# Performance work log

Hardware: AMD Instinct MI355X
Metric: run time of the kernel (lower is better)

Reference implementation:

```python
import jax, jax.numpy as jnp
import numpy as np

R = 6                 # max displacement / padding
D = 2 * R + 1         # window side; D*D = 169 displacements


def setup_inputs() -> dict:
    key = jax.random.key(0)
    k1, k2, k3 = jax.random.split(key, 3)
    b, cf, h, w = 2, 32, 256, 256
    feats_t = jax.random.normal(k1, (b, cf, h, w), jnp.float32)
    feats_r = jax.random.normal(k2, (b, cf, h, w), jnp.float32)
    img_r = jax.random.uniform(k3, (b, 1, h, w), jnp.float32)
    return {"feats_t": feats_t, "feats_r": feats_r, "img_r": img_r}


def _forward(feats_t, feats_r, img_r):
    b, cf, h, w = feats_t.shape
    ci = img_r.shape[1]
    x2p = jnp.pad(feats_r, ((0, 0), (0, 0), (R, R), (R, R)))
    imgp = jnp.pad(img_r, ((0, 0), (0, 0), (R, R), (R, R)))
    # displacement offsets in the same order as the torch double loop (_y outer, _x inner)
    offs = jnp.stack(
        jnp.meshgrid(jnp.arange(D), jnp.arange(D), indexing="ij"), axis=-1
    ).reshape(-1, 2)

    def step(carry, off):
        dy, dx = off[0], off[1]
        win = jax.lax.dynamic_slice(x2p, (0, 0, dy, dx), (b, cf, h, w))
        c = jnp.sum(feats_t * win, axis=1)  # [b, h, w] correlation for this displacement
        iw = jax.lax.dynamic_slice(imgp, (0, 0, dy, dx), (b, ci, h, w))
        return carry, (c, iw)

    _, (corr, imgs) = jax.lax.scan(step, 0, offs)  # corr: [D*D, b, h, w]; imgs: [D*D, b, ci, h, w]
    attn = jax.nn.softmax(corr, axis=0)  # softmax over displacements (torch dim=1 channel axis)
    # weighted sum of shifted reference images -> warped target image
    return jnp.einsum("dbhw,dbchw->bchw", attn, imgs)


def reference(feats_t, feats_r, img_r):
    return _forward(feats_t, feats_r, img_r)
```

## Files before the change

kernel.cpp:

```cpp
#include <hip/hip_runtime.h>
#include <stdint.h>

typedef _Float16 half_t;
typedef _Float16 v4h __attribute__((ext_vector_type(4)));
typedef _Float16 v8h __attribute__((ext_vector_type(8)));
typedef float v4f __attribute__((ext_vector_type(4)));

#define HH 256
#define WW 256
#define HW (HH*WW)
#define TH 32
#define TW 16
#define NROWS (TH+12)
#define NPX   (TW+16)
#define PXS   40
#define RSTEP (NPX*PXS)
#define NTHREADS 1024
#define L2E 1.44269504088896340736f

__global__ __launch_bounds__(NTHREADS, 4)
void corr_recon(const float* __restrict__ ft, const float* __restrict__ fr,
                const float* __restrict__ img, float* __restrict__ out)
{
    __shared__ half_t frl[NROWS * RSTEP];

    const int bid0 = blockIdx.x;
    const int bid  = (bid0 & 7) * 32 + (bid0 >> 3);

    const int b0  = bid >> 7;
    const int rb  = bid & 127;
    const int y0  = (rb >> 4) * TH;
    const int x0t = (rb & 15) * TW;

    const int tid  = threadIdx.x;
    const int lane = tid & 63;
    const int w    = tid >> 6;
    const int n    = lane & 15;
    const int g    = lane >> 4;

    const float* frb = fr  + (size_t)b0 * 32 * HW;
    const float* ftb = ft  + (size_t)b0 * 32 * HW;
    const float* imb = img + (size_t)b0 * HW;

    float iw0r[14], iw1r[14];
    {
        const int gx0  = x0t - 6 + n;
        const int gx1  = gx0 + 16;
        const int gx0c = max(gx0, 0);
        const int gx1c = min(gx1, WW-1);
        const bool okx0 = (gx0 >= 0);
        const bool okx1 = (gx1 < WW);
        #pragma unroll
        for (int u = 0; u < 14; ++u) {
            const int gy  = y0 - 6 + 2*w + u;
            const int gyc = min(max(gy, 0), HH-1);
            const bool oky = (gy == gyc);
            const float v0 = imb[(size_t)gyc * WW + gx0c];
            const float v1 = imb[(size_t)gyc * WW + gx1c];
            iw0r[u] = (oky && okx0) ? v0 : 0.f;
            iw1r[u] = (oky && okx1) ? v1 : 0.f;
        }
    }

    for (int i = tid; i < NROWS * 8 * 8; i += NTHREADS) {
        const int px4 = i & 7;
        const int q   = (i >> 3) & 7;
        const int row = i >> 6;
        const int gy  = y0 - 6 + row;
        const int gx  = x0t - 6 + px4 * 4;
        const int gyc = min(max(gy, 0), HH-1);
        const bool oky = (gy == gyc);
        const float* src = frb + ((size_t)(4*q) * HH + gyc) * WW;
        float t[4][4];
        if (oky && gx >= 0 && gx + 3 < WW) {
            #pragma unroll
            for (int jc = 0; jc < 4; ++jc) {
                float4 v = *(const float4*)(src + (size_t)jc * HW + gx);
                t[jc][0]=v.x; t[jc][1]=v.y; t[jc][2]=v.z; t[jc][3]=v.w;
            }
        } else {
            #pragma unroll
            for (int jc = 0; jc < 4; ++jc)
                #pragma unroll
                for (int e = 0; e < 4; ++e) {
                    int x = gx + e;
                    t[jc][e] = (oky && x >= 0 && x < WW) ? src[(size_t)jc * HW + x] : 0.f;
                }
        }
        const int qo = 8*(q & 3) + 4*(q >> 2);
        #pragma unroll
        for (int jp = 0; jp < 4; ++jp) {
            const int px = px4 * 4 + jp;
            v4h pk;
            pk[0] = (half_t)t[0][jp]; pk[1] = (half_t)t[1][jp];
            pk[2] = (half_t)t[2][jp]; pk[3] = (half_t)t[3][jp];
            *(v4h*)&frl[(row * NPX + px) * PXS + qo] = pk;
        }
    }

    const int y = y0 + 2*w;
    v8h a0, a1;
    {
        const float* fa = ftb + (size_t)y * WW + (x0t + n);
        #pragma unroll
        for (int j = 0; j < 4; ++j) {
            a0[j]   = (half_t)(fa[(size_t)(4*g + j)      * HW] * L2E);
            a0[4+j] = (half_t)(fa[(size_t)(16 + 4*g + j) * HW] * L2E);
            a1[j]   = (half_t)(fa[WW + (size_t)(4*g + j)      * HW] * L2E);
            a1[4+j] = (half_t)(fa[WW + (size_t)(16 + 4*g + j) * HW] * L2E);
        }
    }

    v4f bias0, bias1;
    #pragma unroll
    for (int r = 0; r < 4; ++r) {
        const int m  = 4*g + r;
        const int d0 = n - m;
        const int d1 = 16 + n - m;
        bias0[r] = (d0 >= 0 && d0 <= 12) ? 0.f : -1e4f;
        bias1[r] = (d1 >= 0 && d1 <= 12) ? 0.f : -1e4f;
    }
    const int dm = n - 4*g;

    __syncthreads();

    v4f lp0 = {0,0,0,0}, ap0 = {0,0,0,0};
    v4f lp1 = {0,0,0,0}, ap1 = {0,0,0,0};

    auto STEP = [&](const v8h& a, v4f& lp, v4f& ap,
                    const v8h& B0, const v8h& B1, float iw0, float iw1) {
        v4f c0 = __builtin_amdgcn_mfma_f32_16x16x32_f16(a, B0, bias0, 0, 0, 0);
        v4f c1 = __builtin_amdgcn_mfma_f32_16x16x32_f16(a, B1, bias1, 0, 0, 0);
        #pragma unroll
        for (int r = 0; r < 4; ++r) {
            const bool cond = (dm >= r);
            float cs  = cond ? c0[r] : c1[r];
            float iws = cond ? iw0   : iw1;
            float e = __builtin_amdgcn_exp2f(cs);
            lp[r] += e;
            ap[r] += e * iws;
        }
    };

    const half_t* prd = &frl[(2*w * NPX + n) * PXS + 8*g];
    #pragma unroll
    for (int u = 0; u < 14; ++u) {
        v8h B0 = *(const v8h*)(prd + u*RSTEP);
        v8h B1 = *(const v8h*)(prd + u*RSTEP + 16*PXS);
        if (u <= 12) STEP(a0, lp0, ap0, B0, B1, iw0r[u], iw1r[u]);
        if (u >= 1)  STEP(a1, lp1, ap1, B0, B1, iw0r[u], iw1r[u]);
    }

    #pragma unroll
    for (int r = 0; r < 4; ++r) {
        float l0 = lp0[r], v0 = ap0[r], l1 = lp1[r], v1 = ap1[r];
        l0 += __shfl_xor(l0, 1);  v0 += __shfl_xor(v0, 1);
        l1 += __shfl_xor(l1, 1);  v1 += __shfl_xor(v1, 1);
        l0 += __shfl_xor(l0, 2);  v0 += __shfl_xor(v0, 2);
        l1 += __shfl_xor(l1, 2);  v1 += __shfl_xor(v1, 2);
        l0 += __shfl_xor(l0, 4);  v0 += __shfl_xor(v0, 4);
        l1 += __shfl_xor(l1, 4);  v1 += __shfl_xor(v1, 4);
        l0 += __shfl_xor(l0, 8);  v0 += __shfl_xor(v0, 8);
        l1 += __shfl_xor(l1, 8);  v1 += __shfl_xor(v1, 8);
        lp0[r] = l0; ap0[r] = v0; lp1[r] = l1; ap1[r] = v1;
    }
    if (n < 4) {
        const float l0 = n==0 ? lp0[0] : n==1 ? lp0[1] : n==2 ? lp0[2] : lp0[3];
        const float v0 = n==0 ? ap0[0] : n==1 ? ap0[1] : n==2 ? ap0[2] : ap0[3];
        const float l1 = n==0 ? lp1[0] : n==1 ? lp1[1] : n==2 ? lp1[2] : lp1[3];
        const float v1 = n==0 ? ap1[0] : n==1 ? ap1[1] : n==2 ? ap1[2] : ap1[3];
        float* orow = out + (size_t)b0 * HW + (size_t)y * WW + x0t + 4*g + n;
        orow[0]  = v0 / l0;
        orow[WW] = v1 / l1;
    }
}

extern "C" void kernel_launch(void* const* d_in, const int* in_sizes, int n_in,
                              void* d_out, int out_size, void* d_ws, size_t ws_size,
                              hipStream_t stream)
{
    const float* ft  = (const float*)d_in[0];
    const float* fr  = (const float*)d_in[1];
    const float* img = (const float*)d_in[2];
    float* out = (float*)d_out;
    (void)in_sizes; (void)n_in; (void)out_size; (void)d_ws; (void)ws_size;
    corr_recon<<<256, NTHREADS, 0, stream>>>(ft, fr, img, out);
}
```

Baseline: 19.56 us.

## Drop LDS staging of reference features and load MFMA operands from global memory

Removes the shared-memory tile of fp16 reference features and the block barrier. Each lane now fetches its MFMA B operands straight from global memory, with scalar loads per channel and a cast to fp16 in registers. The tile shrinks to 16 rows with 512 threads, and the grid doubles to 512 blocks to raise parallelism. This avoids the LDS fill and the sync, but it issues many uncoalesced, strided global loads that get re-read across waves and rely on the caches.

```diff
diff --git a/kernel.cpp b/kernel.cpp
--- a/kernel.cpp
+++ b/kernel.cpp
@@ -2,33 +2,26 @@
 #include <stdint.h>
 
 typedef _Float16 half_t;
-typedef _Float16 v4h __attribute__((ext_vector_type(4)));
 typedef _Float16 v8h __attribute__((ext_vector_type(8)));
 typedef float v4f __attribute__((ext_vector_type(4)));
 
 #define HH 256
 #define WW 256
 #define HW (HH*WW)
-#define TH 32
+#define TH 16
 #define TW 16
-#define NROWS (TH+12)
-#define NPX   (TW+16)
-#define PXS   40
-#define RSTEP (NPX*PXS)
-#define NTHREADS 1024
+#define NTHREADS 512
 #define L2E 1.44269504088896340736f
 
 __global__ __launch_bounds__(NTHREADS, 4)
 void corr_recon(const float* __restrict__ ft, const float* __restrict__ fr,
                 const float* __restrict__ img, float* __restrict__ out)
 {
-    __shared__ half_t frl[NROWS * RSTEP];
+    const int bid0 = blockIdx.x;
+    const int bid  = (bid0 & 7) * 64 + (bid0 >> 3);
 
-    const int bid0 = blockIdx.x;
-    const int bid  = (bid0 & 7) * 32 + (bid0 >> 3);
-
-    const int b0  = bid >> 7;
-    const int rb  = bid & 127;
+    const int b0  = bid >> 8;
+    const int rb  = bid & 255;
     const int y0  = (rb >> 4) * TH;
     const int x0t = (rb & 15) * TW;
 
@@ -42,60 +35,23 @@
     const float* ftb = ft  + (size_t)b0 * 32 * HW;
     const float* imb = img + (size_t)b0 * HW;
 
+    const int gx0  = x0t - 6 + n;
+    const int gx1  = gx0 + 16;
+    const int gx0c = max(gx0, 0);
+    const int gx1c = min(gx1, WW-1);
+    const bool okx0 = (gx0 >= 0);
+    const bool okx1 = (gx1 < WW);
+
     float iw0r[14], iw1r[14];
-    {
-        const int gx0  = x0t - 6 + n;
-        const int gx1  = gx0 + 16;
-        const int gx0c = max(gx0, 0);
-        const int gx1c = min(gx1, WW-1);
-        const bool okx0 = (gx0 >= 0);
-        const bool okx1 = (gx1 < WW);
-        #pragma unroll
-        for (int u = 0; u < 14; ++u) {
-            const int gy  = y0 - 6 + 2*w + u;
-            const int gyc = min(max(gy, 0), HH-1);
-            const bool oky = (gy == gyc);
-            const float v0 = imb[(size_t)gyc * WW + gx0c];
-            const float v1 = imb[(size_t)gyc * WW + gx1c];
-            iw0r[u] = (oky && okx0) ? v0 : 0.f;
-            iw1r[u] = (oky && okx1) ? v1 : 0.f;
-        }
-    }
-
-    for (int i = tid; i < NROWS * 8 * 8; i += NTHREADS) {
-        const int px4 = i & 7;
-        const int q   = (i >> 3) & 7;
-        const int row = i >> 6;
-        const int gy  = y0 - 6 + row;
-        const int gx  = x0t - 6 + px4 * 4;
+    #pragma unroll
+    for (int u = 0; u < 14; ++u) {
+        const int gy  = y0 + 2*w - 6 + u;
         const int gyc = min(max(gy, 0), HH-1);
         const bool oky = (gy == gyc);
-        const float* src = frb + ((size_t)(4*q) * HH + gyc) * WW;
-        float t[4][4];
-        if (oky && gx >= 0 && gx + 3 < WW) {
-            #pragma unroll
-            for (int jc = 0; jc < 4; ++jc) {
-                float4 v = *(const float4*)(src + (size_t)jc * HW + gx);
-                t[jc][0]=v.x; t[jc][1]=v.y; t[jc][2]=v.z; t[jc][3]=v.w;
-            }
-        } else {
-            #pragma unroll
-            for (int jc = 0; jc < 4; ++jc)
-                #pragma unroll
-                for (int e = 0; e < 4; ++e) {
-                    int x = gx + e;
-                    t[jc][e] = (oky && x >= 0 && x < WW) ? src[(size_t)jc * HW + x] : 0.f;
-                }
-        }
-        const int qo = 8*(q & 3) + 4*(q >> 2);
-        #pragma unroll
-        for (int jp = 0; jp < 4; ++jp) {
-            const int px = px4 * 4 + jp;
-            v4h pk;
-            pk[0] = (half_t)t[0][jp]; pk[1] = (half_t)t[1][jp];
-            pk[2] = (half_t)t[2][jp]; pk[3] = (half_t)t[3][jp];
-            *(v4h*)&frl[(row * NPX + px) * PXS + qo] = pk;
-        }
+        const float v0 = imb[(size_t)gyc * WW + gx0c];
+        const float v1 = imb[(size_t)gyc * WW + gx1c];
+        iw0r[u] = (oky && okx0) ? v0 : 0.f;
+        iw1r[u] = (oky && okx1) ? v1 : 0.f;
     }
 
     const int y = y0 + 2*w;
@@ -122,8 +78,6 @@
     }
     const int dm = n - 4*g;
 
-    __syncthreads();
-
     v4f lp0 = {0,0,0,0}, ap0 = {0,0,0,0};
     v4f lp1 = {0,0,0,0}, ap1 = {0,0,0,0};
 
@@ -142,11 +96,32 @@
         }
     };
 
-    const half_t* prd = &frl[(2*w * NPX + n) * PXS + 8*g];
+    const float* pb0 = frb + (size_t)(4*g) * HW;
+
     #pragma unroll
     for (int u = 0; u < 14; ++u) {
-        v8h B0 = *(const v8h*)(prd + u*RSTEP);
-        v8h B1 = *(const v8h*)(prd + u*RSTEP + 16*PXS);
+        const int gy  = y0 + 2*w - 6 + u;
+        const int gyc = min(max(gy, 0), HH-1);
+        const bool oky = (gy == gyc);
+        const float* r0 = pb0 + (size_t)gyc * WW;
+
+        float f0[8], f1[8];
+        #pragma unroll
+        for (int j = 0; j < 4; ++j) {
+            f0[j]   = r0[(size_t)j        * HW + gx0c];
+            f0[4+j] = r0[(size_t)(16 + j) * HW + gx0c];
+            f1[j]   = r0[(size_t)j        * HW + gx1c];
+            f1[4+j] = r0[(size_t)(16 + j) * HW + gx1c];
+        }
+        const bool m0 = oky && okx0;
+        const bool m1 = oky && okx1;
+        v8h B0, B1;
+        #pragma unroll
+        for (int j = 0; j < 8; ++j) {
+            B0[j] = (half_t)(m0 ? f0[j] : 0.f);
+            B1[j] = (half_t)(m1 ? f1[j] : 0.f);
+        }
+
         if (u <= 12) STEP(a0, lp0, ap0, B0, B1, iw0r[u], iw1r[u]);
         if (u >= 1)  STEP(a1, lp1, ap1, B0, B1, iw0r[u], iw1r[u]);
     }
@@ -184,5 +159,5 @@
     const float* img = (const float*)d_in[2];
     float* out = (float*)d_out;
     (void)in_sizes; (void)n_in; (void)out_size; (void)d_ws; (void)ws_size;
-    corr_recon<<<256, NTHREADS, 0, stream>>>(ft, fr, img, out);
+    corr_recon<<<512, NTHREADS, 0, stream>>>(ft, fr, img, out);
 }
```

Measured after the change: 74.71 us. 3.82x slower.
